# Performance work log

Measured on AMD Instinct MI355X. Metric: run time of the kernel, lower is better.

The kernel has to match this reference:

```python
import jax, jax.numpy as jnp
import numpy as np

silu = jax.nn.silu
EPS = 1e-5  # GroupNorm eps (torch default)
GROUPS = 8  # split_nums


def conv2d(x, w, b=None, pad=0, groups=1):
    out = jax.lax.conv_general_dilated(
        x, w, window_strides=(1, 1), padding=[(pad, pad), (pad, pad)],
        dimension_numbers=("NCHW", "OIHW", "NCHW"), feature_group_count=groups)
    if b is not None:
        out = out + b[None, :, None, None]
    return out


def group_norm(x, gamma, beta, groups=GROUPS, eps=EPS):
    B, C, H, W = x.shape
    xg = x.reshape(B, groups, C // groups, H, W)
    mu = xg.mean(axis=(2, 3, 4), keepdims=True)
    var = xg.var(axis=(2, 3, 4), keepdims=True)
    xg = (xg - mu) * jax.lax.rsqrt(var + eps)
    x = xg.reshape(B, C, H, W)
    return x * gamma[None, :, None, None] + beta[None, :, None, None]


def setup_inputs() -> dict:
    key = jax.random.key(0)
    ks = jax.random.split(key, 16)
    Ci, Co = 64, 64
    B, H, W = 8, 256, 256
    s = 0.1
    return {
        "x": jax.random.normal(ks[0], (B, Ci, H, W), dtype=jnp.float32),
        "conv1_w": jax.random.normal(ks[1], (Co, Ci, 1, 1), jnp.float32) * s,
        "conv1_b": jnp.zeros((Co,), jnp.float32),
        "dw1_w": jax.random.normal(ks[2], (Co, 1, 1, 1), jnp.float32) * s,
        "dw1_b": jnp.zeros((Co,), jnp.float32),
        "dw2_w": jax.random.normal(ks[3], (Co, 1, 3, 3), jnp.float32) * s,
        "dw2_b": jnp.zeros((Co,), jnp.float32),
        "dw3_w": jax.random.normal(ks[4], (Co, 1, 5, 5), jnp.float32) * s,
        "dw3_b": jnp.zeros((Co,), jnp.float32),
        "pw_w": jax.random.normal(ks[5], (Ci, 3 * Co, 1, 1), jnp.float32) * s,
        "pw_b": jnp.zeros((Ci,), jnp.float32),
        "ca_w1": jax.random.normal(ks[6], (Ci // 8, Ci, 1, 1), jnp.float32) * s,
        "ca_w2": jax.random.normal(ks[7], (Ci, Ci // 8, 1, 1), jnp.float32) * s,
        "sa_w": jax.random.normal(ks[8], (1, 2, 7, 7), jnp.float32) * s,
        "sa_b": jnp.zeros((1,), jnp.float32),
        "gn_g": jnp.ones((Ci,), jnp.float32),
        "gn_b": jnp.zeros((Ci,), jnp.float32),
    }


def reference(x, conv1_w, conv1_b, dw1_w, dw1_b, dw2_w, dw2_b, dw3_w, dw3_b,
              pw_w, pw_b, ca_w1, ca_w2, sa_w, sa_b, gn_g, gn_b):
    Co = conv1_w.shape[0]
    x_init = x
    # multi-scale depthwise branch
    h = silu(conv2d(x, conv1_w, conv1_b))
    h1 = conv2d(h, dw1_w, dw1_b, pad=0, groups=Co)
    h2 = conv2d(h, dw2_w, dw2_b, pad=1, groups=Co)
    h3 = conv2d(h, dw3_w, dw3_b, pad=2, groups=Co)
    h = jnp.concatenate([h1, h2, h3], axis=1)
    h = silu(conv2d(h, pw_w, pw_b)) + x_init
    h = silu(h)
    # CBAM: channel attention
    avg_p = h.mean(axis=(2, 3), keepdims=True)   # [B,C,1,1]
    max_p = h.max(axis=(2, 3), keepdims=True)
    mlp = lambda p: conv2d(jax.nn.relu(conv2d(p, ca_w1)), ca_w2)
    ca = silu(mlp(avg_p) + mlp(max_p))
    out = ca * h
    # CBAM: spatial attention
    sp = jnp.concatenate([out.mean(axis=1, keepdims=True),
                          out.max(axis=1, keepdims=True)], axis=1)  # [B,2,H,W]
    sa = silu(conv2d(sp, sa_w, sa_b, pad=3))
    out = sa * out
    # GroupNorm + SiLU
    return silu(group_norm(out, gn_g, gn_b))
```

## Files before the change

### kernel.cpp

```cpp
#include <hip/hip_runtime.h>
#include <math.h>

#define B_ 8
#define C_ 64
#define W_ 256
#define HWSZ 65536
#define NPIX (B_*HWSZ)
#define NELEM (B_*C_*HWSZ)

#define WS_H     0
#define WS_SP    33554432
#define WS_STATS 34603008
#define S_SUM    0
#define S_MAXU   512
#define S_GSUM   1024
#define S_GSQ    1088
#define S_CA     1152
#define S_GMEAN  1664
#define S_GRSTD  1728
#define WS_PWT   (WS_STATS + 2048)

__device__ __forceinline__ float siluf(float v) {
    return v / (1.0f + __expf(-v));
}

__device__ __forceinline__ unsigned fenc(float f) {
    unsigned u = __float_as_uint(f);
    return (u & 0x80000000u) ? ~u : (u | 0x80000000u);
}
__device__ __forceinline__ float fdec(unsigned u) {
    return (u & 0x80000000u) ? __uint_as_float(u & 0x7fffffffu) : __uint_as_float(~u);
}

__global__ __launch_bounds__(256) void k_tr(const float* __restrict__ pw,
                                            float* __restrict__ pwT) {
    int i = blockIdx.x * 256 + threadIdx.x;
    if (i < 12288) {
        int co = i / 192;
        int k  = i - co * 192;
        pwT[k * 64 + co] = pw[i];
    }
}

__global__ __launch_bounds__(256) void k_conv1(const float* __restrict__ x,
                                               const float* __restrict__ w,
                                               const float* __restrict__ bias,
                                               float* __restrict__ h) {
    int p  = blockIdx.x * 256 + threadIdx.x;
    int b  = p >> 16;
    int hw = p & (HWSZ - 1);
    const float* xp = x + ((size_t)b << 22) + hw;
    float xr[64];
#pragma unroll
    for (int ci = 0; ci < 64; ++ci) xr[ci] = xp[(size_t)ci << 16];
    float* hp = h + ((size_t)b << 22) + hw;
    const float4* w4 = (const float4*)w;
    for (int co = 0; co < 64; ++co) {
        float acc = bias[co];
#pragma unroll
        for (int q = 0; q < 16; ++q) {
            float4 wv = w4[co * 16 + q];
            acc += wv.x * xr[4*q] + wv.y * xr[4*q+1] + wv.z * xr[4*q+2] + wv.w * xr[4*q+3];
        }
        hp[(size_t)co << 16] = siluf(acc);
    }
}

__global__ __launch_bounds__(256) void k_msdw(
    const float* __restrict__ h, const float* __restrict__ x,
    const float* __restrict__ dw1w, const float* __restrict__ dw1b,
    const float* __restrict__ dw2w, const float* __restrict__ dw2b,
    const float* __restrict__ dw3w, const float* __restrict__ dw3b,
    const float* __restrict__ pwT, const float* __restrict__ pwb,
    float* __restrict__ hact,
    float* __restrict__ stat_sum, unsigned* __restrict__ stat_max) {
    __shared__ float ht[2][400];
    __shared__ float red_s[4][64];
    __shared__ float red_m[4][64];
    int tid = threadIdx.x;
    int b   = blockIdx.y;
    int x0  = (blockIdx.x & 15) << 4;
    int y0  = (blockIdx.x >> 4) << 4;
    int tx  = tid & 15, ty = tid >> 4;
    int hw  = ((y0 + ty) << 8) + (x0 + tx);

    float acc[64];
#pragma unroll
    for (int i = 0; i < 64; ++i) acc[i] = 0.f;

    {
        const float* hc = h + ((size_t)(b * 64) << 16);
        for (int i = tid; i < 400; i += 256) {
            int ly = i / 20, lx = i - ly * 20;
            int gy = y0 - 2 + ly, gx = x0 - 2 + lx;
            ht[0][i] = ((unsigned)gy < 256u && (unsigned)gx < 256u) ? hc[(gy << 8) + gx] : 0.f;
        }
    }
    __syncthreads();

    for (int c = 0; c < 64; ++c) {
        int cur = c & 1;
        if (c < 63) {
            const float* hc = h + ((size_t)(b * 64 + c + 1) << 16);
            int i0 = tid, i1 = tid + 256;
            int ly = i0 / 20, lx = i0 - ly * 20;
            int gy = y0 - 2 + ly, gx = x0 - 2 + lx;
            float v0 = ((unsigned)gy < 256u && (unsigned)gx < 256u) ? hc[(gy << 8) + gx] : 0.f;
            ht[cur ^ 1][i0] = v0;
            if (i1 < 400) {
                int ly1 = i1 / 20, lx1 = i1 - ly1 * 20;
                int gy1 = y0 - 2 + ly1, gx1 = x0 - 2 + lx1;
                float v1 = ((unsigned)gy1 < 256u && (unsigned)gx1 < 256u) ? hc[(gy1 << 8) + gx1] : 0.f;
                ht[cur ^ 1][i1] = v1;
            }
        }
        float w3r[25], w2r[9];
#pragma unroll
        for (int k = 0; k < 25; ++k) w3r[k] = dw3w[c * 25 + k];
#pragma unroll
        for (int k = 0; k < 9; ++k)  w2r[k] = dw2w[c * 9 + k];
        float w1c = dw1w[c], b1c = dw1b[c], b2c = dw2b[c], b3c = dw3b[c];

        float d2 = b2c, d3 = b3c, center = 0.f;
#pragma unroll
        for (int dy = 0; dy < 5; ++dy) {
#pragma unroll
            for (int dx = 0; dx < 5; ++dx) {
                float hv = ht[cur][(ty + dy) * 20 + tx + dx];
                d3 += hv * w3r[dy * 5 + dx];
                if (dy >= 1 && dy <= 3 && dx >= 1 && dx <= 3)
                    d2 += hv * w2r[(dy - 1) * 3 + (dx - 1)];
                if (dy == 2 && dx == 2) center = hv;
            }
        }
        float d1 = center * w1c + b1c;

        const float4* wp = (const float4*)pwT;
#pragma unroll
        for (int q = 0; q < 16; ++q) {
            float4 wa = wp[(c << 4) + q];
            float4 wb = wp[((64 + c) << 4) + q];
            float4 wc = wp[((128 + c) << 4) + q];
            acc[4*q+0] += wa.x * d1 + wb.x * d2 + wc.x * d3;
            acc[4*q+1] += wa.y * d1 + wb.y * d2 + wc.y * d3;
            acc[4*q+2] += wa.z * d1 + wb.z * d2 + wc.z * d3;
            acc[4*q+3] += wa.w * d1 + wb.w * d2 + wc.w * d3;
        }
        __syncthreads();
    }

    int lane = tid & 63, wid = tid >> 6;
    const float* xpix = x + ((size_t)b << 22) + hw;
    float* op = hact + ((size_t)b << 22) + hw;
#pragma unroll
    for (int co = 0; co < 64; ++co) {
        float v = siluf(acc[co] + pwb[co]);
        v += xpix[(size_t)co << 16];
        v = siluf(v);
        op[(size_t)co << 16] = v;
        float s = v, m = v;
#pragma unroll
        for (int off = 32; off > 0; off >>= 1) {
            s += __shfl_xor(s, off);
            m = fmaxf(m, __shfl_xor(m, off));
        }
        if (lane == 0) { red_s[wid][co] = s; red_m[wid][co] = m; }
    }
    __syncthreads();
    if (tid < 64) {
        float S = red_s[0][tid] + red_s[1][tid] + red_s[2][tid] + red_s[3][tid];
        float M = fmaxf(fmaxf(red_m[0][tid], red_m[1][tid]),
                        fmaxf(red_m[2][tid], red_m[3][tid]));
        atomicAdd(&stat_sum[b * 64 + tid], S);
        atomicMax(&stat_max[b * 64 + tid], fenc(M));
    }
}

__global__ __launch_bounds__(64) void k_ca(const float* __restrict__ ssum,
                                           const unsigned* __restrict__ smax,
                                           const float* __restrict__ w1,
                                           const float* __restrict__ w2,
                                           float* __restrict__ ca) {
    __shared__ float avg[64], mxs[64], t1[16];
    int b = blockIdx.x, c = threadIdx.x;
    avg[c] = ssum[b * 64 + c] * (1.0f / 65536.0f);
    mxs[c] = fdec(smax[b * 64 + c]);
    __syncthreads();
    if (c < 16) {
        int j = c & 7;
        const float* src = (c < 8) ? avg : mxs;
        float t = 0.f;
        for (int k = 0; k < 64; ++k) t += w1[j * 64 + k] * src[k];
        t1[c] = fmaxf(t, 0.f);
    }
    __syncthreads();
    float ua = 0.f, um = 0.f;
#pragma unroll
    for (int j = 0; j < 8; ++j) {
        ua += w2[c * 8 + j] * t1[j];
        um += w2[c * 8 + j] * t1[8 + j];
    }
    ca[b * 64 + c] = siluf(ua + um);
}

__global__ __launch_bounds__(256) void k_spool(const float* __restrict__ hact,
                                               const float* __restrict__ ca,
                                               float* __restrict__ sp) {
    int t  = blockIdx.x * 256 + threadIdx.x;
    int p4 = t << 2;
    int b  = p4 >> 16;
    int hw = p4 & (HWSZ - 1);
    const float4* hp = (const float4*)(hact + ((size_t)b << 22) + hw);
    const float*  cab = ca + b * 64;
    float4 mn = {0.f, 0.f, 0.f, 0.f};
    float4 mx = {-3e38f, -3e38f, -3e38f, -3e38f};
#pragma unroll
    for (int c = 0; c < 64; ++c) {
        float cc = cab[c];
        float4 hv = hp[(size_t)c << 14];
        float vx = hv.x * cc, vy = hv.y * cc, vz = hv.z * cc, vw = hv.w * cc;
        mn.x += vx; mn.y += vy; mn.z += vz; mn.w += vw;
        mx.x = fmaxf(mx.x, vx); mx.y = fmaxf(mx.y, vy);
        mx.z = fmaxf(mx.z, vz); mx.w = fmaxf(mx.w, vw);
    }
    mn.x *= (1.f/64.f); mn.y *= (1.f/64.f); mn.z *= (1.f/64.f); mn.w *= (1.f/64.f);
    *(float4*)(sp + ((size_t)(b * 2) << 16) + hw) = mn;
    *(float4*)(sp + ((size_t)(b * 2) << 16) + HWSZ + hw) = mx;
}

__global__ __launch_bounds__(256) void k_sattn(const float* __restrict__ hact,
                                               const float* __restrict__ sp,
                                               const float* __restrict__ ca,
                                               const float* __restrict__ saw,
                                               const float* __restrict__ sab,
                                               float* __restrict__ out,
                                               float* __restrict__ gsum,
                                               float* __restrict__ gsq) {
    __shared__ float rs[4][16];
    int tid = threadIdx.x;
    int t   = blockIdx.x * 256 + tid;
    int p4  = t << 2;
    int b   = p4 >> 16;
    int hw  = p4 & (HWSZ - 1);
    int y   = hw >> 8, xx = hw & 255;
    float a0 = sab[0], a1 = a0, a2 = a0, a3 = a0;
#pragma unroll
    for (int ch = 0; ch < 2; ++ch) {
        const float* spb = sp + ((size_t)(b * 2 + ch) << 16);
#pragma unroll
        for (int dy = 0; dy < 7; ++dy) {
            int gy = y + dy - 3;
            bool vr = (unsigned)gy < 256u;
            const float* rowp = spb + (gy << 8);
            float r[10];
#pragma unroll
            for (int k = 0; k < 10; ++k) {
                int gx = xx + k - 3;
                r[k] = (vr && (unsigned)gx < 256u) ? rowp[gx] : 0.f;
            }
#pragma unroll
            for (int k = 0; k < 7; ++k) {
                float wv = saw[ch * 49 + dy * 7 + k];
                a0 += r[k] * wv; a1 += r[k+1] * wv; a2 += r[k+2] * wv; a3 += r[k+3] * wv;
            }
        }
    }
    float s0 = siluf(a0), s1 = siluf(a1), s2 = siluf(a2), s3 = siluf(a3);
    const float* cab = ca + b * 64;
    const float4* hp = (const float4*)(hact + ((size_t)b << 22) + hw);
    float4* op = (float4*)(out + ((size_t)b << 22) + hw);
    float gs[8], gq[8];
#pragma unroll
    for (int g = 0; g < 8; ++g) { gs[g] = 0.f; gq[g] = 0.f; }
#pragma unroll
    for (int c = 0; c < 64; ++c) {
        float cc = cab[c];
        float4 hv = hp[(size_t)c << 14];
        float4 o;
        o.x = hv.x * cc * s0; o.y = hv.y * cc * s1;
        o.z = hv.z * cc * s2; o.w = hv.w * cc * s3;
        op[(size_t)c << 14] = o;
        int g = c >> 3;
        gs[g] += o.x + o.y + o.z + o.w;
        gq[g] += o.x*o.x + o.y*o.y + o.z*o.z + o.w*o.w;
    }
    int lane = tid & 63, wid = tid >> 6;
#pragma unroll
    for (int g = 0; g < 8; ++g) {
#pragma unroll
        for (int off = 32; off > 0; off >>= 1) {
            gs[g] += __shfl_xor(gs[g], off);
            gq[g] += __shfl_xor(gq[g], off);
        }
    }
    if (lane == 0) {
#pragma unroll
        for (int g = 0; g < 8; ++g) { rs[wid][g] = gs[g]; rs[wid][8 + g] = gq[g]; }
    }
    __syncthreads();
    if (tid < 16) {
        float v = rs[0][tid] + rs[1][tid] + rs[2][tid] + rs[3][tid];
        int g = tid & 7;
        if (tid < 8) atomicAdd(&gsum[b * 8 + g], v);
        else         atomicAdd(&gsq[b * 8 + g], v);
    }
}

__global__ __launch_bounds__(64) void k_gnstat(const float* __restrict__ gsum,
                                               const float* __restrict__ gsq,
                                               float* __restrict__ gmean,
                                               float* __restrict__ grstd) {
    int t = threadIdx.x;
    const float n = 524288.0f;
    float mu  = gsum[t] / n;
    float var = gsq[t] / n - mu * mu;
    gmean[t] = mu;
    grstd[t] = rsqrtf(var + 1e-5f);
}

__global__ __launch_bounds__(256) void k_gn(float* __restrict__ out,
                                            const float* __restrict__ gmean,
                                            const float* __restrict__ grstd,
                                            const float* __restrict__ gw,
                                            const float* __restrict__ gb) {
    int t    = blockIdx.x * 256 + threadIdx.x;
    int base = t << 2;
    int c    = (base >> 16) & 63;
    int b    = base >> 22;
    int tg   = b * 8 + (c >> 3);
    float rstd  = grstd[tg];
    float gamma = gw[c] * rstd;
    float beta  = gb[c] - gmean[tg] * gamma;
    float4 v = ((float4*)out)[t];
    v.x = siluf(v.x * gamma + beta);
    v.y = siluf(v.y * gamma + beta);
    v.z = siluf(v.z * gamma + beta);
    v.w = siluf(v.w * gamma + beta);
    ((float4*)out)[t] = v;
}

extern "C" void kernel_launch(void* const* d_in, const int* in_sizes, int n_in,
                              void* d_out, int out_size, void* d_ws, size_t ws_size,
                              hipStream_t stream) {
    const float* x    = (const float*)d_in[0];
    const float* c1w  = (const float*)d_in[1];
    const float* c1b  = (const float*)d_in[2];
    const float* dw1w = (const float*)d_in[3];
    const float* dw1b = (const float*)d_in[4];
    const float* dw2w = (const float*)d_in[5];
    const float* dw2b = (const float*)d_in[6];
    const float* dw3w = (const float*)d_in[7];
    const float* dw3b = (const float*)d_in[8];
    const float* pww  = (const float*)d_in[9];
    const float* pwb  = (const float*)d_in[10];
    const float* caw1 = (const float*)d_in[11];
    const float* caw2 = (const float*)d_in[12];
    const float* saw  = (const float*)d_in[13];
    const float* sab  = (const float*)d_in[14];
    const float* gng  = (const float*)d_in[15];
    const float* gnb  = (const float*)d_in[16];

    float* out   = (float*)d_out;
    float* ws    = (float*)d_ws;
    float* hact  = ws + WS_H;
    float* sp    = ws + WS_SP;
    float* stats = ws + WS_STATS;
    float* ssum  = stats + S_SUM;
    unsigned* smax = (unsigned*)(stats + S_MAXU);
    float* gsum  = stats + S_GSUM;
    float* gsq   = stats + S_GSQ;
    float* cav   = stats + S_CA;
    float* gmean = stats + S_GMEAN;
    float* grstd = stats + S_GRSTD;
    float* pwT   = ws + WS_PWT;

    hipMemsetAsync(stats, 0, 1152 * sizeof(float), stream);
    k_tr<<<48, 256, 0, stream>>>(pww, pwT);
    k_conv1<<<NPIX / 256, 256, 0, stream>>>(x, c1w, c1b, out);
    dim3 g2(256, 8);
    k_msdw<<<g2, 256, 0, stream>>>(out, x, dw1w, dw1b, dw2w, dw2b, dw3w, dw3b,
                                   pwT, pwb, hact, ssum, smax);
    k_ca<<<8, 64, 0, stream>>>(ssum, smax, caw1, caw2, cav);
    k_spool<<<NPIX / 1024, 256, 0, stream>>>(hact, cav, sp);
    k_sattn<<<NPIX / 1024, 256, 0, stream>>>(hact, sp, cav, saw, sab, out, gsum, gsq);
    k_gnstat<<<1, 64, 0, stream>>>(gsum, gsq, gmean, grstd);
    k_gn<<<NELEM / 1024, 256, 0, stream>>>(out, gmean, grstd, gng, gnb);
}
```

Before: 841.7 us.

## Process two channels per iteration with register-prefetched halo tiles in msdw kernel

The depthwise/pointwise fused kernel now loads halo tiles for two channels at a time. Global offsets are precomputed once per thread, and the loads for the next pair go into registers before compute. They are written to shared memory only after compute, so memory latency overlaps the convolution math. This halves the number of barriers per block and removes the per-iteration index division, at the cost of more registers and twice the shared tile storage.

```diff
diff --git a/kernel.cpp b/kernel.cpp
--- a/kernel.cpp
+++ b/kernel.cpp
@@ -74,7 +74,8 @@
     const float* __restrict__ pwT, const float* __restrict__ pwb,
     float* __restrict__ hact,
     float* __restrict__ stat_sum, unsigned* __restrict__ stat_max) {
-    __shared__ float ht[2][400];
+    __shared__ float htA[800];
+    __shared__ float htB[800];
     __shared__ float red_s[4][64];
     __shared__ float red_m[4][64];
     int tid = threadIdx.x;
@@ -84,69 +85,95 @@
     int tx  = tid & 15, ty = tid >> 4;
     int hw  = ((y0 + ty) << 8) + (x0 + tx);
 
+    int s_goff[4];
+#pragma unroll
+    for (int s = 0; s < 4; ++s) {
+        int j = tid + (s << 8);
+        int ch  = (j >= 400) ? 1 : 0;
+        int off = j - (ch ? 400 : 0);
+        int ly = off / 20, lx = off - ly * 20;
+        int gy = y0 - 2 + ly, gx = x0 - 2 + lx;
+        s_goff[s] = (j < 800 && (unsigned)gy < 256u && (unsigned)gx < 256u)
+                        ? ((ch << 16) | (gy << 8) | gx) : -1;
+    }
+
     float acc[64];
 #pragma unroll
     for (int i = 0; i < 64; ++i) acc[i] = 0.f;
 
     {
-        const float* hc = h + ((size_t)(b * 64) << 16);
-        for (int i = tid; i < 400; i += 256) {
-            int ly = i / 20, lx = i - ly * 20;
-            int gy = y0 - 2 + ly, gx = x0 - 2 + lx;
-            ht[0][i] = ((unsigned)gy < 256u && (unsigned)gx < 256u) ? hc[(gy << 8) + gx] : 0.f;
+        const float* hb = h + ((size_t)(b * 64) << 16);
+#pragma unroll
+        for (int s = 0; s < 4; ++s) {
+            int j = tid + (s << 8);
+            if (j < 800) {
+                float v = (s_goff[s] >= 0) ? hb[s_goff[s]] : 0.f;
+                htA[j] = v;
+            }
         }
     }
     __syncthreads();
 
-    for (int c = 0; c < 64; ++c) {
-        int cur = c & 1;
-        if (c < 63) {
-            const float* hc = h + ((size_t)(b * 64 + c + 1) << 16);
-            int i0 = tid, i1 = tid + 256;
-            int ly = i0 / 20, lx = i0 - ly * 20;
-            int gy = y0 - 2 + ly, gx = x0 - 2 + lx;
-            float v0 = ((unsigned)gy < 256u && (unsigned)gx < 256u) ? hc[(gy << 8) + gx] : 0.f;
-            ht[cur ^ 1][i0] = v0;
-            if (i1 < 400) {
-                int ly1 = i1 / 20, lx1 = i1 - ly1 * 20;
-                int gy1 = y0 - 2 + ly1, gx1 = x0 - 2 + lx1;
-                float v1 = ((unsigned)gy1 < 256u && (unsigned)gx1 < 256u) ? hc[(gy1 << 8) + gx1] : 0.f;
-                ht[cur ^ 1][i1] = v1;
+    float* cur = htA;
+    float* nxt = htB;
+    const float4* wp = (const float4*)pwT;
+
+    for (int it = 0; it < 32; ++it) {
+        float pf0 = 0.f, pf1 = 0.f, pf2 = 0.f, pf3 = 0.f;
+        if (it < 31) {
+            const float* hn = h + ((size_t)(b * 64 + 2 * it + 2) << 16);
+            pf0 = (s_goff[0] >= 0) ? hn[s_goff[0]] : 0.f;
+            pf1 = (s_goff[1] >= 0) ? hn[s_goff[1]] : 0.f;
+            pf2 = (s_goff[2] >= 0) ? hn[s_goff[2]] : 0.f;
+            if (tid < 32) pf3 = (s_goff[3] >= 0) ? hn[s_goff[3]] : 0.f;
+        }
+
+#pragma unroll
+        for (int half = 0; half < 2; ++half) {
+            int c = (it << 1) + half;
+            const float* tile = cur + half * 400 + ty * 20 + tx;
+
+            float w3r[25], w2r[9];
+#pragma unroll
+            for (int k = 0; k < 25; ++k) w3r[k] = dw3w[c * 25 + k];
+#pragma unroll
+            for (int k = 0; k < 9; ++k)  w2r[k] = dw2w[c * 9 + k];
+            float w1c = dw1w[c], b1c = dw1b[c], b2c = dw2b[c], b3c = dw3b[c];
+
+            float d2 = b2c, d3 = b3c, center = 0.f;
+#pragma unroll
+            for (int dy = 0; dy < 5; ++dy) {
+#pragma unroll
+                for (int dx = 0; dx < 5; ++dx) {
+                    float hv = tile[dy * 20 + dx];
+                    d3 += hv * w3r[dy * 5 + dx];
+                    if (dy >= 1 && dy <= 3 && dx >= 1 && dx <= 3)
+                        d2 += hv * w2r[(dy - 1) * 3 + (dx - 1)];
+                    if (dy == 2 && dx == 2) center = hv;
+                }
             }
-        }
-        float w3r[25], w2r[9];
-#pragma unroll
-        for (int k = 0; k < 25; ++k) w3r[k] = dw3w[c * 25 + k];
-#pragma unroll
-        for (int k = 0; k < 9; ++k)  w2r[k] = dw2w[c * 9 + k];
-        float w1c = dw1w[c], b1c = dw1b[c], b2c = dw2b[c], b3c = dw3b[c];
-
-        float d2 = b2c, d3 = b3c, center = 0.f;
-#pragma unroll
-        for (int dy = 0; dy < 5; ++dy) {
-#pragma unroll
-            for (int dx = 0; dx < 5; ++dx) {
-                float hv = ht[cur][(ty + dy) * 20 + tx + dx];
-                d3 += hv * w3r[dy * 5 + dx];
-                if (dy >= 1 && dy <= 3 && dx >= 1 && dx <= 3)
-                    d2 += hv * w2r[(dy - 1) * 3 + (dx - 1)];
-                if (dy == 2 && dx == 2) center = hv;
+            float d1 = center * w1c + b1c;
+
+#pragma unroll
+            for (int q = 0; q < 16; ++q) {
+                float4 wa = wp[(c << 4) + q];
+                float4 wb = wp[((64 + c) << 4) + q];
+                float4 wc = wp[((128 + c) << 4) + q];
+                acc[4*q+0] += wa.x * d1 + wb.x * d2 + wc.x * d3;
+                acc[4*q+1] += wa.y * d1 + wb.y * d2 + wc.y * d3;
+                acc[4*q+2] += wa.z * d1 + wb.z * d2 + wc.z * d3;
+                acc[4*q+3] += wa.w * d1 + wb.w * d2 + wc.w * d3;
             }
         }
-        float d1 = center * w1c + b1c;
-
-        const float4* wp = (const float4*)pwT;
-#pragma unroll
-        for (int q = 0; q < 16; ++q) {
-            float4 wa = wp[(c << 4) + q];
-            float4 wb = wp[((64 + c) << 4) + q];
-            float4 wc = wp[((128 + c) << 4) + q];
-            acc[4*q+0] += wa.x * d1 + wb.x * d2 + wc.x * d3;
-            acc[4*q+1] += wa.y * d1 + wb.y * d2 + wc.y * d3;
-            acc[4*q+2] += wa.z * d1 + wb.z * d2 + wc.z * d3;
-            acc[4*q+3] += wa.w * d1 + wb.w * d2 + wc.w * d3;
+
+        if (it < 31) {
+            nxt[tid]       = pf0;
+            nxt[tid + 256] = pf1;
+            nxt[tid + 512] = pf2;
+            if (tid < 32) nxt[tid + 768] = pf3;
         }
         __syncthreads();
+        float* t = cur; cur = nxt; nxt = t;
     }
 
     int lane = tid & 63, wid = tid >> 6;
```

New measurement: 1.395 ms. 65.7% more time.
